# Performance work log

Hardware: AMD Instinct MI355X
Metric: run time of the kernel (lower is better)

Reference implementation:

```python
import jax, jax.numpy as jnp
import numpy as np
from jax import lax

NPOINT = 1024
K = 32
EPS = 1e-5  # BatchNorm eps (eval mode, running stats)


def _fps(xyz, npoint):
    """Farthest point sampling. xyz: [B,N,3] -> idx [B,npoint] (int32).
    Deterministic start at index 0 (torch version starts at a random index)."""
    B, N, _ = xyz.shape
    barange = jnp.arange(B)

    def step(carry, _):
        distance, farthest = carry
        centroid = xyz[barange, farthest]                    # [B,3]
        d = jnp.sum((xyz - centroid[:, None, :]) ** 2, -1)   # [B,N]
        distance = jnp.minimum(distance, d)
        new_far = jnp.argmax(distance, axis=-1).astype(jnp.int32)
        return (distance, new_far), farthest

    init = (jnp.full((B, N), 1e10, dtype=xyz.dtype), jnp.zeros((B,), jnp.int32))
    _, centroids = lax.scan(step, init, None, length=npoint)  # [npoint,B]
    return centroids.T                                        # [B,npoint]


def _square_distance(src, dst):
    # src [B,M,3], dst [B,N,3] -> [B,M,N]
    return (jnp.sum(src ** 2, -1)[:, :, None]
            - 2.0 * jnp.einsum('bmc,bnc->bmn', src, dst)
            + jnp.sum(dst ** 2, -1)[:, None, :])


def _gather(p, idx):
    # p [B,N,C], idx [B,...] -> [B,...,C]
    return jax.vmap(lambda pb, ib: pb[ib])(p, idx)


def _mlp_layer(x, w, cb, g, b, m, v):
    # x [B,S,K,Cin]; Conv2d 1x1 == channel matmul, then eval-mode BN, ReLU
    x = jnp.einsum('bskc,oc->bsko', x, w) + cb
    x = (x - m) * (g / jnp.sqrt(v + EPS)) + b
    return jax.nn.relu(x)


def _forward(xyz, points, w0, cb0, g0, b0, m0, v0,
             w1, cb1, g1, b1, m1, v1, w2, cb2, g2, b2, m2, v2):
    fps_idx = _fps(xyz, NPOINT)                       # [B,S]
    new_xyz = _gather(xyz, fps_idx)                   # [B,S,3]
    dists = _square_distance(new_xyz, xyz)            # [B,S,N]
    _, nn_idx = lax.top_k(-dists, K)                  # [B,S,K]
    grouped_xyz = _gather(xyz, nn_idx)                # [B,S,K,3]
    grouped_xyz_norm = grouped_xyz - new_xyz[:, :, None, :]
    grouped_pts = _gather(points, nn_idx)             # [B,S,K,C]
    x = jnp.concatenate([grouped_xyz_norm, grouped_pts], axis=-1)  # [B,S,K,3+C]
    x = _mlp_layer(x, w0, cb0, g0, b0, m0, v0)
    x = _mlp_layer(x, w1, cb1, g1, b1, m1, v1)
    x = _mlp_layer(x, w2, cb2, g2, b2, m2, v2)
    new_points = jnp.max(x, axis=2)                   # max over K -> [B,S,Cout]
    return new_xyz, jnp.transpose(new_points, (0, 2, 1))  # [B,Cout,S]


def setup_inputs() -> dict:
    key = jax.random.key(0)
    ks = jax.random.split(key, 8)
    B, N, C = 16, 4096, 64
    inp = {
        'xyz': jax.random.normal(ks[0], (B, N, 3), jnp.float32),
        'points': jax.random.normal(ks[1], (B, N, C), jnp.float32),
    }
    channels = [(3 + C, 64), (64, 64), (64, 128)]
    for li, (ci, co) in enumerate(channels):
        inp[f'w{li}'] = jax.random.normal(ks[2 + li], (co, ci), jnp.float32) * 0.05
        inp[f'cb{li}'] = jnp.zeros((co,), jnp.float32)
        inp[f'g{li}'] = jnp.ones((co,), jnp.float32)
        inp[f'b{li}'] = jnp.zeros((co,), jnp.float32)
        inp[f'm{li}'] = jnp.zeros((co,), jnp.float32)
        inp[f'v{li}'] = jnp.ones((co,), jnp.float32)
    return inp


def reference(xyz, points, w0, cb0, g0, b0, m0, v0,
              w1, cb1, g1, b1, m1, v1, w2, cb2, g2, b2, m2, v2):
    return _forward(xyz, points, w0, cb0, g0, b0, m0, v0,
                    w1, cb1, g1, b1, m1, v1, w2, cb2, g2, b2, m2, v2)
```

## Files before the change

kernel.cpp:

```cpp
#include <hip/hip_runtime.h>
#include <math.h>

#define NPTS 4096
#define NB 16
#define NS 1024
#define KNB 32
#define CPTS 64

#define FLAG_OFF_B  0
#define CNT_OFF_B   64
#define PUBC_OFF_B  128
#define WFRAG_ELEMS 18432
#define NGROUPS     2048

typedef __attribute__((ext_vector_type(8))) short short8;
typedef __attribute__((ext_vector_type(4))) float f32x4;

__device__ __forceinline__ short f2bf(float f) {
  unsigned u = __float_as_uint(f);
  unsigned r = (u + 0x7fffu + ((u >> 16) & 1u)) >> 16;
  return (short)r;
}

template <int CTRL>
__device__ __forceinline__ int dppmov(int cur) {
  return __builtin_amdgcn_update_dpp(cur, cur, CTRL, 0xF, 0xF, false);
}
template <int CTRL>
__device__ __forceinline__ void dpp_min_u64(unsigned& hi, unsigned& lo) {
  unsigned nhi = (unsigned)dppmov<CTRL>((int)hi);
  unsigned nlo = (unsigned)dppmov<CTRL>((int)lo);
  bool lt = (nhi < hi) || (nhi == hi && nlo < lo);
  hi = lt ? nhi : hi;
  lo = lt ? nlo : lo;
}
template <int CTRL>
__device__ __forceinline__ void dpp_max_u64(unsigned& hi, unsigned& lo) {
  unsigned nhi = (unsigned)dppmov<CTRL>((int)hi);
  unsigned nlo = (unsigned)dppmov<CTRL>((int)lo);
  bool gt = (nhi > hi) || (nhi == hi && nlo > lo);
  hi = gt ? nhi : hi;
  lo = gt ? nlo : lo;
}
template <int CTRL>
__device__ __forceinline__ void dpp_fmax(float& m) {
  m = fmaxf(m, __int_as_float(dppmov<CTRL>(__float_as_int(m))));
}
template <int CTRL>
__device__ __forceinline__ void dpp_umin(unsigned& v) {
  unsigned o = (unsigned)dppmov<CTRL>((int)v);
  v = (o < v) ? o : v;
}

#define XSTR 104
__global__ __launch_bounds__(512, 2) void fused_kernel(
    const float* __restrict__ xyz, const float* __restrict__ points,
    const float* __restrict__ w0, const float* __restrict__ cb0, const float* __restrict__ g0,
    const float* __restrict__ b0, const float* __restrict__ m0, const float* __restrict__ v0,
    const float* __restrict__ w1, const float* __restrict__ cb1, const float* __restrict__ g1,
    const float* __restrict__ b1, const float* __restrict__ m1, const float* __restrict__ v1,
    const float* __restrict__ w2, const float* __restrict__ cb2, const float* __restrict__ g2,
    const float* __restrict__ b2, const float* __restrict__ m2, const float* __restrict__ v2,
    char* __restrict__ wsb, float* __restrict__ newxyz, float* __restrict__ outp) {
  struct FpsSh {
    float4 sxyz4[NPTS];
    float4 centL[NS];
    unsigned long long part[2][8];
  };
  struct WorkerSh {
    short Wlds[WFRAG_ELEMS];
    union {
      unsigned long long slist[2][4096];
      short X[8][32 * XSTR];
    } u;
    unsigned long long wl[2][128];
    int nnL[8][KNB];
    float biasL[256];
    float pubq[8][3];
    unsigned gshare;
  };
  __shared__ union { FpsSh f; WorkerSh w; } sh;

  const int t = threadIdx.x;
  const int lane = t & 63;
  const int wave = t >> 6;
  unsigned* flagp = (unsigned*)(wsb + FLAG_OFF_B);
  unsigned* cntp  = (unsigned*)(wsb + CNT_OFF_B);
  float* pubC = (float*)(wsb + PUBC_OFF_B);

  if (blockIdx.x < NB) {
    const int b = blockIdx.x;
    const float* xb = xyz + (size_t)b * NPTS * 3;
    float* outb = newxyz + (size_t)b * NS * 3;

    for (int i = t; i < NPTS; i += 512)
      sh.f.sxyz4[i] = make_float4(xb[i * 3 + 0], xb[i * 3 + 1], xb[i * 3 + 2], 0.f);

    float px[8], py[8], pz[8], dist[8];
#pragma unroll
    for (int j = 0; j < 8; ++j) {
      int n = t + 512 * j;
      px[j] = xb[n * 3 + 0];
      py[j] = xb[n * 3 + 1];
      pz[j] = xb[n * 3 + 2];
      dist[j] = 1e10f;
    }
    __syncthreads();
    float cx = sh.f.sxyz4[0].x, cy = sh.f.sxyz4[0].y, cz = sh.f.sxyz4[0].z;
    if (t == 0) sh.f.centL[0] = sh.f.sxyz4[0];

    for (int it = 1; it < NS; ++it) {
      const int buf = it & 1;
      float dm[8];
#pragma unroll
      for (int j = 0; j < 8; ++j) {
        float dx = __fsub_rn(px[j], cx);
        float dy = __fsub_rn(py[j], cy);
        float dz = __fsub_rn(pz[j], cz);
        float d  = __fadd_rn(__fadd_rn(__fmul_rn(dx, dx), __fmul_rn(dy, dy)), __fmul_rn(dz, dz));
        float v  = fminf(dist[j], d);
        dist[j] = v;
        dm[j] = v;
      }
      float m = fmaxf(fmaxf(fmaxf(dm[0], dm[1]), fmaxf(dm[2], dm[3])),
                      fmaxf(fmaxf(dm[4], dm[5]), fmaxf(dm[6], dm[7])));
      dpp_fmax<0xB1>(m);  dpp_fmax<0x4E>(m);  dpp_fmax<0x141>(m);
      dpp_fmax<0x140>(m); dpp_fmax<0x142>(m); dpp_fmax<0x143>(m);
      float M = __int_as_float(__builtin_amdgcn_readlane(__float_as_int(m), 63));
      unsigned idxl = 0xFFFFFFFFu;
#pragma unroll
      for (int j = 7; j >= 0; --j) idxl = (dm[j] == M) ? (unsigned)(t + 512 * j) : idxl;
      dpp_umin<0xB1>(idxl);  dpp_umin<0x4E>(idxl);  dpp_umin<0x141>(idxl);
      dpp_umin<0x140>(idxl); dpp_umin<0x142>(idxl); dpp_umin<0x143>(idxl);
      if (lane == 63)
        sh.f.part[buf][wave] = ((unsigned long long)__float_as_uint(M) << 32) | (unsigned)(~idxl);
      __syncthreads();
      unsigned long long k0 = sh.f.part[buf][lane & 7];
      unsigned khi = (unsigned)(k0 >> 32), klo = (unsigned)k0;
      dpp_max_u64<0xB1>(khi, klo);
      dpp_max_u64<0x4E>(khi, klo);
      dpp_max_u64<0x141>(khi, klo);
      int bi = (int)(~klo) & 4095;
      float4 c4 = sh.f.sxyz4[bi];
      cx = c4.x; cy = c4.y; cz = c4.z;
      if (t == 0) sh.f.centL[it] = c4;
      if ((it & 31) == 31 && wave == 0) {
        if (lane == 0)
          __hip_atomic_store(&flagp[b], (unsigned)(it - 31), __ATOMIC_RELEASE, __HIP_MEMORY_SCOPE_AGENT);
        if (lane < 32) {
          int ci = it - 31 + lane;
          float4 cc = sh.f.centL[ci];
          float* dst = pubC + ((size_t)b * NS + ci) * 3;
          __hip_atomic_store(dst + 0, cc.x, __ATOMIC_RELAXED, __HIP_MEMORY_SCOPE_AGENT);
          __hip_atomic_store(dst + 1, cc.y, __ATOMIC_RELAXED, __HIP_MEMORY_SCOPE_AGENT);
          __hip_atomic_store(dst + 2, cc.z, __ATOMIC_RELAXED, __HIP_MEMORY_SCOPE_AGENT);
        }
      }
    }
    if (wave == 0 && lane == 0)
      __hip_atomic_store(&flagp[b], (unsigned)NS, __ATOMIC_RELEASE, __HIP_MEMORY_SCOPE_AGENT);
    __syncthreads();
    const float* cf = (const float*)sh.f.centL;
    for (int i = t; i < NS * 3; i += 512) {
      int p = i / 3, c = i - p * 3;
      outb[i] = cf[p * 4 + c];
    }
  }

  __syncthreads();
  for (int i = t; i < WFRAG_ELEMS; i += 512) {
    int g = i >> 9, ln = (i >> 3) & 63, j = i & 7;
    int l, nt, s;
    if (g < 12)      { l = 0; nt = g / 3;  s = g % 3; }
    else if (g < 20) { l = 1; int gg = g - 12; nt = gg >> 1; s = gg & 1; }
    else             { l = 2; int gg = g - 20; nt = gg >> 1; s = gg & 1; }
    int n = nt * 16 + (ln & 15);
    int k = s * 32 + ((ln >> 4) << 3) + j;
    float val = 0.f;
    if (l == 0) { if (k < 67) val = w0[n * 67 + k] * (g0[n] / sqrtf(v0[n] + 1e-5f)); }
    else if (l == 1) { val = w1[n * 64 + k] * (g1[n] / sqrtf(v1[n] + 1e-5f)); }
    else { val = w2[n * 64 + k] * (g2[n] / sqrtf(v2[n] + 1e-5f)); }
    sh.w.Wlds[i] = f2bf(val);
  }
  if (t < 256) {
    int o = t;
    float bv;
    if (o < 64)       { float sc = g0[o] / sqrtf(v0[o] + 1e-5f); bv = (cb0[o] - m0[o]) * sc + b0[o]; }
    else if (o < 128) { int c = o - 64;  float sc = g1[c] / sqrtf(v1[c] + 1e-5f); bv = (cb1[c] - m1[c]) * sc + b1[c]; }
    else              { int c = o - 128; float sc = g2[c] / sqrtf(v2[c] + 1e-5f); bv = (cb2[c] - m2[c]) * sc + b2[c]; }
    sh.w.biasL[o] = bv;
  }
  const int team = t >> 8, tt = t & 255;

  for (;;) {
    __syncthreads();
    if (t == 0) sh.w.gshare = atomicAdd(cntp, 1u);
    __syncthreads();
    unsigned g = sh.w.gshare;
    if (g >= NGROUPS) break;
    const int b = (int)(g & 15u);
    const int s0 = (int)(g >> 4) << 3;

    if (t == 0) {
      unsigned need = (unsigned)(s0 + 8);
      for (;;) {
        unsigned f = __hip_atomic_load(&flagp[b], __ATOMIC_ACQUIRE, __HIP_MEMORY_SCOPE_AGENT);
        if (f >= need) break;
        __builtin_amdgcn_s_sleep(8);
      }
    }
    __syncthreads();
    if (t < 24)
      sh.w.pubq[t / 3][t % 3] = __hip_atomic_load(
          &pubC[((size_t)b * NS + s0 + t / 3) * 3 + (t % 3)],
          __ATOMIC_RELAXED, __HIP_MEMORY_SCOPE_AGENT);
    __syncthreads();

    const float* xb = xyz + (size_t)b * NPTS * 3;

    for (int sub = 0; sub < 4; ++sub) {
      const int qi = team * 4 + sub;
      float qx = sh.w.pubq[qi][0], qy = sh.w.pubq[qi][1], qz = sh.w.pubq[qi][2];
      float s2 = __fadd_rn(__fadd_rn(__fmul_rn(qx, qx), __fmul_rn(qy, qy)), __fmul_rn(qz, qz));
      unsigned long long key[16];
#pragma unroll
      for (int j = 0; j < 16; ++j) {
        int n = tt + 256 * j;
        float px = xb[n * 3], py = xb[n * 3 + 1], pz = xb[n * 3 + 2];
        float n2 = __fadd_rn(__fadd_rn(__fmul_rn(px, px), __fmul_rn(py, py)), __fmul_rn(pz, pz));
        float dt = __fadd_rn(__fadd_rn(__fmul_rn(qx, px), __fmul_rn(qy, py)), __fmul_rn(qz, pz));
        float d  = __fadd_rn(__fsub_rn(s2, __fmul_rn(2.0f, dt)), n2);
        unsigned u = __float_as_uint(d);
        u ^= (0x80000000u | (unsigned)((int)u >> 31));
        key[j] = ((unsigned long long)u << 32) | (unsigned)n;
      }
#pragma unroll
      for (int p = 1; p < 16; p <<= 1) {
#pragma unroll
        for (int k = p; k >= 1; k >>= 1) {
#pragma unroll
          for (int j = k % p; j + k < 16; j += 2 * k) {
#pragma unroll
            for (int i = 0; i < k; ++i) {
              if (i + j + k < 16 && (i + j) / (2 * p) == (i + j + k) / (2 * p)) {
                unsigned long long ka = key[i + j], kb = key[i + j + k];
                unsigned long long mn = ka < kb ? ka : kb;
                unsigned long long mx = ka < kb ? kb : ka;
                key[i + j] = mn; key[i + j + k] = mx;
              }
            }
          }
        }
      }
#pragma unroll
      for (int i = 0; i < 16; ++i) sh.w.u.slist[team][i * 256 + tt] = key[i];

      unsigned long long head = key[0];
      unsigned long long nxt  = key[1];
      unsigned p = 1;
      for (int r = 0; r < KNB; ++r) {
        unsigned hi = (unsigned)(head >> 32), lo = (unsigned)head;
        dpp_min_u64<0xB1>(hi, lo);
        dpp_min_u64<0x4E>(hi, lo);
        dpp_min_u64<0x141>(hi, lo);
        dpp_min_u64<0x140>(hi, lo);
        dpp_min_u64<0x142>(hi, lo);
        dpp_min_u64<0x143>(hi, lo);
        unsigned whi = (unsigned)__builtin_amdgcn_readlane((int)hi, 63);
        unsigned wlo = (unsigned)__builtin_amdgcn_readlane((int)lo, 63);
        unsigned long long wkey = ((unsigned long long)whi << 32) | wlo;
        if ((tt & 63) == 0) sh.w.wl[team][(tt >> 6) * 32 + r] = wkey;
        if (head == wkey) {
          head = (p < 16) ? nxt : 0xFFFFFFFFFFFFFFFFull;
          unsigned pn = p + 1;
          nxt = sh.w.u.slist[team][(pn < 16 ? pn : 15) * 256 + tt];
          p = pn;
        }
      }
      __syncthreads();
      if (tt < 128) {
        unsigned long long mykey = sh.w.wl[team][tt];
        int gr = 0;
#pragma unroll 8
        for (int i = 0; i < 128; ++i) gr += (sh.w.wl[team][i] < mykey) ? 1 : 0;
        if (gr < KNB) sh.w.nnL[qi][gr] = (int)(mykey & 0xFFFFFFFFull);
      }
      __syncthreads();
    }

    {
      const int qi = wave;
      const int s = s0 + qi;
      float qx = sh.w.pubq[qi][0], qy = sh.w.pubq[qi][1], qz = sh.w.pubq[qi][2];
      const float* pb = points + (size_t)b * NPTS * CPTS;
      const float* bias = sh.w.biasL;
      short* X = sh.w.u.X[qi];

      {
        int r = lane & 31, half = lane >> 5;
        int idx = sh.w.nnL[qi][r];
        const float* prow = pb + (size_t)idx * CPTS;
#pragma unroll
        for (int i = 0; i < 48; ++i) {
          int c = half * 48 + i;
          float v;
          if (c < 3) {
            float qc = (c == 0) ? qx : ((c == 1) ? qy : qz);
            v = __fsub_rn(xb[idx * 3 + c], qc);
          } else if (c < 67) {
            v = prow[c - 3];
          } else {
            v = 0.f;
          }
          X[r * XSTR + c] = f2bf(v);
        }
      }

      const int ml = lane & 15, quad = lane >> 4;
      const short8* Wf = (const short8*)sh.w.Wlds;

      short8 a0[2][3];
#pragma unroll
      for (int m2 = 0; m2 < 2; ++m2)
#pragma unroll
        for (int s3 = 0; s3 < 3; ++s3)
          a0[m2][s3] = *(const short8*)&X[(m2 * 16 + ml) * XSTR + s3 * 32 + quad * 8];
      f32x4 acc0[2][4];
#pragma unroll
      for (int m2 = 0; m2 < 2; ++m2)
#pragma unroll
        for (int nt = 0; nt < 4; ++nt) {
          f32x4 c = {0.f, 0.f, 0.f, 0.f};
#pragma unroll
          for (int s3 = 0; s3 < 3; ++s3)
            c = __builtin_amdgcn_mfma_f32_16x16x32_bf16(a0[m2][s3], Wf[(nt * 3 + s3) * 64 + lane], c, 0, 0, 0);
          acc0[m2][nt] = c;
        }
#pragma unroll
      for (int m2 = 0; m2 < 2; ++m2)
#pragma unroll
        for (int nt = 0; nt < 4; ++nt) {
          int ch = nt * 16 + ml;
          float bv = bias[ch];
#pragma unroll
          for (int r4 = 0; r4 < 4; ++r4) {
            float y = fmaxf(acc0[m2][nt][r4] + bv, 0.f);
            int m = quad * 4 + r4;
            int sK = ch >> 5, qq = (ch >> 3) & 3, jj = ch & 7;
            X[((m2 * 2 + sK) * 64 + qq * 16 + m) * 8 + jj] = f2bf(y);
          }
        }

      short8 a1[2][2];
#pragma unroll
      for (int m2 = 0; m2 < 2; ++m2)
#pragma unroll
        for (int sK = 0; sK < 2; ++sK)
          a1[m2][sK] = *(const short8*)&X[((m2 * 2 + sK) * 64 + lane) * 8];
      f32x4 acc1[2][4];
#pragma unroll
      for (int m2 = 0; m2 < 2; ++m2)
#pragma unroll
        for (int nt = 0; nt < 4; ++nt) {
          f32x4 c = {0.f, 0.f, 0.f, 0.f};
#pragma unroll
          for (int sK = 0; sK < 2; ++sK)
            c = __builtin_amdgcn_mfma_f32_16x16x32_bf16(a1[m2][sK], Wf[(12 + nt * 2 + sK) * 64 + lane], c, 0, 0, 0);
          acc1[m2][nt] = c;
        }
#pragma unroll
      for (int m2 = 0; m2 < 2; ++m2)
#pragma unroll
        for (int nt = 0; nt < 4; ++nt) {
          int ch = nt * 16 + ml;
          float bv = bias[64 + ch];
#pragma unroll
          for (int r4 = 0; r4 < 4; ++r4) {
            float y = fmaxf(acc1[m2][nt][r4] + bv, 0.f);
            int m = quad * 4 + r4;
            int sK = ch >> 5, qq = (ch >> 3) & 3, jj = ch & 7;
            X[((m2 * 2 + sK) * 64 + qq * 16 + m) * 8 + jj] = f2bf(y);
          }
        }

      short8 a2[2][2];
#pragma unroll
      for (int m2 = 0; m2 < 2; ++m2)
#pragma unroll
        for (int sK = 0; sK < 2; ++sK)
          a2[m2][sK] = *(const short8*)&X[((m2 * 2 + sK) * 64 + lane) * 8];
#pragma unroll
      for (int nt = 0; nt < 8; ++nt) {
        f32x4 c0 = {0.f, 0.f, 0.f, 0.f}, c1 = {0.f, 0.f, 0.f, 0.f};
        short8 w0f = Wf[(20 + nt * 2 + 0) * 64 + lane];
        short8 w1f = Wf[(20 + nt * 2 + 1) * 64 + lane];
        c0 = __builtin_amdgcn_mfma_f32_16x16x32_bf16(a2[0][0], w0f, c0, 0, 0, 0);
        c0 = __builtin_amdgcn_mfma_f32_16x16x32_bf16(a2[0][1], w1f, c0, 0, 0, 0);
        c1 = __builtin_amdgcn_mfma_f32_16x16x32_bf16(a2[1][0], w0f, c1, 0, 0, 0);
        c1 = __builtin_amdgcn_mfma_f32_16x16x32_bf16(a2[1][1], w1f, c1, 0, 0, 0);
        float bv = bias[128 + nt * 16 + ml];
        float m = -1.f;
#pragma unroll
        for (int r4 = 0; r4 < 4; ++r4) {
          m = fmaxf(m, fmaxf(c0[r4] + bv, 0.f));
          m = fmaxf(m, fmaxf(c1[r4] + bv, 0.f));
        }
        m = fmaxf(m, __shfl_xor(m, 16, 64));
        m = fmaxf(m, __shfl_xor(m, 32, 64));
        if (lane < 16) outp[((size_t)b * 128 + nt * 16 + lane) * NS + s] = m;
      }
    }
  }
}

extern "C" void kernel_launch(void* const* d_in, const int* in_sizes, int n_in,
                              void* d_out, int out_size, void* d_ws, size_t ws_size,
                              hipStream_t stream) {
  const float* xyz    = (const float*)d_in[0];
  const float* points = (const float*)d_in[1];
  const float* w0  = (const float*)d_in[2];
  const float* cb0 = (const float*)d_in[3];
  const float* g0  = (const float*)d_in[4];
  const float* b0  = (const float*)d_in[5];
  const float* m0  = (const float*)d_in[6];
  const float* v0  = (const float*)d_in[7];
  const float* w1  = (const float*)d_in[8];
  const float* cb1 = (const float*)d_in[9];
  const float* g1  = (const float*)d_in[10];
  const float* b1  = (const float*)d_in[11];
  const float* m1  = (const float*)d_in[12];
  const float* v1  = (const float*)d_in[13];
  const float* w2  = (const float*)d_in[14];
  const float* cb2 = (const float*)d_in[15];
  const float* g2  = (const float*)d_in[16];
  const float* b2  = (const float*)d_in[17];
  const float* m2  = (const float*)d_in[18];
  const float* v2  = (const float*)d_in[19];

  char*  wsb    = (char*)d_ws;
  float* newxyz = (float*)d_out;
  float* outp   = (float*)d_out + (size_t)NB * NS * 3;

  hipMemsetAsync(wsb, 0, 128, stream);
  fused_kernel<<<256, 512, 0, stream>>>(
      xyz, points, w0, cb0, g0, b0, m0, v0, w1, cb1, g1, b1, m1, v1,
      w2, cb2, g2, b2, m2, v2, wsb, newxyz, outp);
}
```

Measured before the change: 904.7 us.

## Replace per-block sorted KNN merge with per-wave threshold-filter selection

Each wave now claims its own query through a global atomic counter, replacing block-wide groups of 8 queries and the `__syncthreads`-heavy scheduling. The 32 nearest neighbours are found by a new threshold method. Each lane keeps its minimum key, a cross-lane bitonic sort picks the 32nd-smallest lane minimum as a threshold, and a second distance pass pushes keys at or below it into a 256-entry LDS buffer, which is then rank-sorted. This replaces the register bitonic sort and the 32-round DPP merge, at the cost of computing distances twice. If more than 256 points fall under the threshold the buffer truncates and neighbours may be dropped.

```diff
diff --git a/kernel.cpp b/kernel.cpp
--- a/kernel.cpp
+++ b/kernel.cpp
@@ -11,7 +11,8 @@
 #define CNT_OFF_B   64
 #define PUBC_OFF_B  128
 #define WFRAG_ELEMS 18432
-#define NGROUPS     2048
+#define NUNITS      16384
+#define CAP         256
 
 typedef __attribute__((ext_vector_type(8))) short short8;
 typedef __attribute__((ext_vector_type(4))) float f32x4;
@@ -25,14 +26,6 @@
 template <int CTRL>
 __device__ __forceinline__ int dppmov(int cur) {
   return __builtin_amdgcn_update_dpp(cur, cur, CTRL, 0xF, 0xF, false);
-}
-template <int CTRL>
-__device__ __forceinline__ void dpp_min_u64(unsigned& hi, unsigned& lo) {
-  unsigned nhi = (unsigned)dppmov<CTRL>((int)hi);
-  unsigned nlo = (unsigned)dppmov<CTRL>((int)lo);
-  bool lt = (nhi < hi) || (nhi == hi && nlo < lo);
-  hi = lt ? nhi : hi;
-  lo = lt ? nlo : lo;
 }
 template <int CTRL>
 __device__ __forceinline__ void dpp_max_u64(unsigned& hi, unsigned& lo) {
@@ -69,15 +62,11 @@
   };
   struct WorkerSh {
     short Wlds[WFRAG_ELEMS];
-    union {
-      unsigned long long slist[2][4096];
-      short X[8][32 * XSTR];
-    } u;
-    unsigned long long wl[2][128];
+    short X[8][32 * XSTR];
+    unsigned long long cand[8][CAP];
     int nnL[8][KNB];
     float biasL[256];
-    float pubq[8][3];
-    unsigned gshare;
+    unsigned cnt[8];
   };
   __shared__ union { FpsSh f; WorkerSh w; } sh;
 
@@ -190,111 +179,104 @@
     else              { int c = o - 128; float sc = g2[c] / sqrtf(v2[c] + 1e-5f); bv = (cb2[c] - m2[c]) * sc + b2[c]; }
     sh.w.biasL[o] = bv;
   }
-  const int team = t >> 8, tt = t & 255;
+  __syncthreads();
+
+  unsigned long long* cand = sh.w.cand[wave];
 
   for (;;) {
-    __syncthreads();
-    if (t == 0) sh.w.gshare = atomicAdd(cntp, 1u);
-    __syncthreads();
-    unsigned g = sh.w.gshare;
-    if (g >= NGROUPS) break;
-    const int b = (int)(g & 15u);
-    const int s0 = (int)(g >> 4) << 3;
-
-    if (t == 0) {
-      unsigned need = (unsigned)(s0 + 8);
-      for (;;) {
-        unsigned f = __hip_atomic_load(&flagp[b], __ATOMIC_ACQUIRE, __HIP_MEMORY_SCOPE_AGENT);
-        if (f >= need) break;
-        __builtin_amdgcn_s_sleep(8);
-      }
-    }
-    __syncthreads();
-    if (t < 24)
-      sh.w.pubq[t / 3][t % 3] = __hip_atomic_load(
-          &pubC[((size_t)b * NS + s0 + t / 3) * 3 + (t % 3)],
-          __ATOMIC_RELAXED, __HIP_MEMORY_SCOPE_AGENT);
-    __syncthreads();
+    unsigned u = 0;
+    if (lane == 0) u = atomicAdd(cntp, 1u);
+    u = (unsigned)__builtin_amdgcn_readfirstlane((int)u);
+    if (u >= NUNITS) break;
+    const int b = (int)(u & 15u);
+    const int s = (int)(u >> 4);
+
+    {
+      unsigned need = (unsigned)s + 1u;
+      while (__hip_atomic_load(&flagp[b], __ATOMIC_ACQUIRE, __HIP_MEMORY_SCOPE_AGENT) < need)
+        __builtin_amdgcn_s_sleep(64);
+    }
+    const float* qcp = pubC + ((size_t)b * NS + s) * 3;
+    float qx = __hip_atomic_load(qcp + 0, __ATOMIC_RELAXED, __HIP_MEMORY_SCOPE_AGENT);
+    float qy = __hip_atomic_load(qcp + 1, __ATOMIC_RELAXED, __HIP_MEMORY_SCOPE_AGENT);
+    float qz = __hip_atomic_load(qcp + 2, __ATOMIC_RELAXED, __HIP_MEMORY_SCOPE_AGENT);
 
     const float* xb = xyz + (size_t)b * NPTS * 3;
-
-    for (int sub = 0; sub < 4; ++sub) {
-      const int qi = team * 4 + sub;
-      float qx = sh.w.pubq[qi][0], qy = sh.w.pubq[qi][1], qz = sh.w.pubq[qi][2];
-      float s2 = __fadd_rn(__fadd_rn(__fmul_rn(qx, qx), __fmul_rn(qy, qy)), __fmul_rn(qz, qz));
-      unsigned long long key[16];
-#pragma unroll
-      for (int j = 0; j < 16; ++j) {
-        int n = tt + 256 * j;
-        float px = xb[n * 3], py = xb[n * 3 + 1], pz = xb[n * 3 + 2];
-        float n2 = __fadd_rn(__fadd_rn(__fmul_rn(px, px), __fmul_rn(py, py)), __fmul_rn(pz, pz));
-        float dt = __fadd_rn(__fadd_rn(__fmul_rn(qx, px), __fmul_rn(qy, py)), __fmul_rn(qz, pz));
-        float d  = __fadd_rn(__fsub_rn(s2, __fmul_rn(2.0f, dt)), n2);
-        unsigned u = __float_as_uint(d);
-        u ^= (0x80000000u | (unsigned)((int)u >> 31));
-        key[j] = ((unsigned long long)u << 32) | (unsigned)n;
-      }
-#pragma unroll
-      for (int p = 1; p < 16; p <<= 1) {
-#pragma unroll
-        for (int k = p; k >= 1; k >>= 1) {
-#pragma unroll
-          for (int j = k % p; j + k < 16; j += 2 * k) {
-#pragma unroll
-            for (int i = 0; i < k; ++i) {
-              if (i + j + k < 16 && (i + j) / (2 * p) == (i + j + k) / (2 * p)) {
-                unsigned long long ka = key[i + j], kb = key[i + j + k];
-                unsigned long long mn = ka < kb ? ka : kb;
-                unsigned long long mx = ka < kb ? kb : ka;
-                key[i + j] = mn; key[i + j + k] = mx;
-              }
-            }
-          }
-        }
-      }
-#pragma unroll
-      for (int i = 0; i < 16; ++i) sh.w.u.slist[team][i * 256 + tt] = key[i];
-
-      unsigned long long head = key[0];
-      unsigned long long nxt  = key[1];
-      unsigned p = 1;
-      for (int r = 0; r < KNB; ++r) {
-        unsigned hi = (unsigned)(head >> 32), lo = (unsigned)head;
-        dpp_min_u64<0xB1>(hi, lo);
-        dpp_min_u64<0x4E>(hi, lo);
-        dpp_min_u64<0x141>(hi, lo);
-        dpp_min_u64<0x140>(hi, lo);
-        dpp_min_u64<0x142>(hi, lo);
-        dpp_min_u64<0x143>(hi, lo);
-        unsigned whi = (unsigned)__builtin_amdgcn_readlane((int)hi, 63);
-        unsigned wlo = (unsigned)__builtin_amdgcn_readlane((int)lo, 63);
-        unsigned long long wkey = ((unsigned long long)whi << 32) | wlo;
-        if ((tt & 63) == 0) sh.w.wl[team][(tt >> 6) * 32 + r] = wkey;
-        if (head == wkey) {
-          head = (p < 16) ? nxt : 0xFFFFFFFFFFFFFFFFull;
-          unsigned pn = p + 1;
-          nxt = sh.w.u.slist[team][(pn < 16 ? pn : 15) * 256 + tt];
-          p = pn;
-        }
-      }
-      __syncthreads();
-      if (tt < 128) {
-        unsigned long long mykey = sh.w.wl[team][tt];
-        int gr = 0;
-#pragma unroll 8
-        for (int i = 0; i < 128; ++i) gr += (sh.w.wl[team][i] < mykey) ? 1 : 0;
-        if (gr < KNB) sh.w.nnL[qi][gr] = (int)(mykey & 0xFFFFFFFFull);
-      }
-      __syncthreads();
-    }
+    float s2 = __fadd_rn(__fadd_rn(__fmul_rn(qx, qx), __fmul_rn(qy, qy)), __fmul_rn(qz, qz));
+
+    unsigned long long mkey = 0xFFFFFFFFFFFFFFFFull;
+#pragma unroll 4
+    for (int j = 0; j < 64; ++j) {
+      int n = j * 64 + lane;
+      float px = xb[n * 3], py = xb[n * 3 + 1], pz = xb[n * 3 + 2];
+      float n2 = __fadd_rn(__fadd_rn(__fmul_rn(px, px), __fmul_rn(py, py)), __fmul_rn(pz, pz));
+      float dt = __fadd_rn(__fadd_rn(__fmul_rn(qx, px), __fmul_rn(qy, py)), __fmul_rn(qz, pz));
+      float d  = __fadd_rn(__fsub_rn(s2, __fmul_rn(2.0f, dt)), n2);
+      unsigned uu = __float_as_uint(d);
+      uu ^= (0x80000000u | (unsigned)((int)uu >> 31));
+      unsigned long long key = ((unsigned long long)uu << 32) | (unsigned)n;
+      mkey = key < mkey ? key : mkey;
+    }
+
+    {
+      unsigned mh = (unsigned)(mkey >> 32), ml2 = (unsigned)mkey;
+#pragma unroll
+      for (int k = 2; k <= 64; k <<= 1) {
+#pragma unroll
+        for (int j = k >> 1; j >= 1; j >>= 1) {
+          unsigned oh = (unsigned)__shfl_xor((int)mh, j, 64);
+          unsigned ol = (unsigned)__shfl_xor((int)ml2, j, 64);
+          bool up = (lane & k) == 0;
+          bool lower = (lane & j) == 0;
+          bool omin = (oh < mh) || (oh == mh && ol < ml2);
+          bool keep_o = (lower == up) ? omin : !omin;
+          mh = keep_o ? oh : mh;
+          ml2 = keep_o ? ol : ml2;
+        }
+      }
+      unsigned th = (unsigned)__builtin_amdgcn_readlane((int)mh, 31);
+      unsigned tl = (unsigned)__builtin_amdgcn_readlane((int)ml2, 31);
+      mkey = ((unsigned long long)th << 32) | tl;
+    }
+    const unsigned long long tau = mkey;
+
+    if (lane == 0) sh.w.cnt[wave] = 0;
+    asm volatile("s_waitcnt lgkmcnt(0)" ::: "memory");
+#pragma unroll 4
+    for (int j = 0; j < 64; ++j) {
+      int n = j * 64 + lane;
+      float px = xb[n * 3], py = xb[n * 3 + 1], pz = xb[n * 3 + 2];
+      float n2 = __fadd_rn(__fadd_rn(__fmul_rn(px, px), __fmul_rn(py, py)), __fmul_rn(pz, pz));
+      float dt = __fadd_rn(__fadd_rn(__fmul_rn(qx, px), __fmul_rn(qy, py)), __fmul_rn(qz, pz));
+      float d  = __fadd_rn(__fsub_rn(s2, __fmul_rn(2.0f, dt)), n2);
+      unsigned uu = __float_as_uint(d);
+      uu ^= (0x80000000u | (unsigned)((int)uu >> 31));
+      unsigned long long key = ((unsigned long long)uu << 32) | (unsigned)n;
+      if (key <= tau) {
+        unsigned pos = atomicAdd(&sh.w.cnt[wave], 1u);
+        if (pos < CAP) cand[pos] = key;
+      }
+    }
+    asm volatile("s_waitcnt lgkmcnt(0)" ::: "memory");
+    unsigned cn = sh.w.cnt[wave];
+    if (cn > CAP) cn = CAP;
+
+    for (unsigned base = 0; base < cn; base += 64) {
+      unsigned i = base + (unsigned)lane;
+      unsigned long long ki = (i < cn) ? cand[i] : 0xFFFFFFFFFFFFFFFFull;
+      int rank = 0;
+#pragma unroll 4
+      for (unsigned c2 = 0; c2 < cn; ++c2)
+        rank += (cand[c2] < ki) ? 1 : 0;
+      if (i < cn && rank < KNB) sh.w.nnL[wave][rank] = (int)(unsigned)(ki & 0xFFFFFFFFull);
+    }
+    asm volatile("s_waitcnt lgkmcnt(0)" ::: "memory");
 
     {
       const int qi = wave;
-      const int s = s0 + qi;
-      float qx = sh.w.pubq[qi][0], qy = sh.w.pubq[qi][1], qz = sh.w.pubq[qi][2];
       const float* pb = points + (size_t)b * NPTS * CPTS;
       const float* bias = sh.w.biasL;
-      short* X = sh.w.u.X[qi];
+      short* X = sh.w.X[qi];
 
       {
         int r = lane & 31, half = lane >> 5;
```

Measured after the change: 955.3 us. +5.6%, slower.
